# Performance work log

Measured on AMD Instinct MI355X. Metric: run time of the kernel, lower is better.

The kernel has to match this reference:

```python
import jax, jax.numpy as jnp
import numpy as np

H, W = 128, 128          # input_shape
OUT_H, OUT_W = 64, 64    # output_shape -> n_samples = 4096


def setup_inputs() -> dict:
    key = jax.random.key(0)
    k1, k2, k3 = jax.random.split(key, 3)
    activations = jax.random.normal(k1, (8, H, W), dtype=jnp.float32)
    mu = jax.random.uniform(k2, (OUT_H * OUT_W, 2), dtype=jnp.float32)
    sigma = jax.random.uniform(k3, (OUT_H * OUT_W, 2), dtype=jnp.float32)
    return {"activations": activations, "mu": mu, "sigma": sigma}


def reference(activations, mu, sigma):
    # coordinate grid: arange(dim)/dim per axis, range [0, 1)
    gh = jnp.arange(H, dtype=jnp.float32) / H          # [H]
    gw = jnp.arange(W, dtype=jnp.float32) / W          # [W]
    inv2s2 = 1.0 / (2.0 * jnp.square(sigma))           # [N, 2]
    # separable exponent: sum over dims splits into h-part + w-part
    eh = jnp.square(gh[:, None] - mu[None, :, 0]) * inv2s2[None, :, 0]  # [H, N]
    ew = jnp.square(gw[:, None] - mu[None, :, 1]) * inv2s2[None, :, 1]  # [W, N]
    pdf = jnp.exp(-(eh[:, None, :] + ew[None, :, :]))  # [H, W, N]
    # mean over spatial dims of pdf * activations (fused contraction)
    corr = jnp.einsum('bhw,hwn->bn', activations, pdf) / (H * W)  # [B, N]
    return corr.reshape(activations.shape[0], OUT_H, OUT_W)
```

## Files before the change

### kernel.cpp

```cpp
#include <hip/hip_runtime.h>

#define NOUT 4096
#define TN 32

typedef short bf16x8 __attribute__((ext_vector_type(8)));
typedef float f32x4  __attribute__((ext_vector_type(4)));

__device__ __forceinline__ unsigned short f2bf(float x) {
    unsigned u = __float_as_uint(x);
    u = (u + 0x7fffu + ((u >> 16) & 1u)) >> 16;
    return (unsigned short)u;
}
__device__ __forceinline__ float bf2f(unsigned short h) {
    return __uint_as_float(((unsigned)h) << 16);
}

__global__ __launch_bounds__(256) void gauss_mfma_kernel(
    const float* __restrict__ act,
    const float* __restrict__ mu,
    const float* __restrict__ sigma,
    float* __restrict__ out)
{
    __shared__ unsigned short EwH[32][136];
    __shared__ unsigned short EwL[32][136];
    __shared__ float4 musig[32];
    __shared__ float  red[4][32];

    const int t    = threadIdx.x;
    const int wv   = t >> 6;
    const int lane = t & 63;
    const int lm   = lane & 15;
    const int lg   = lane >> 4;
    const int n0   = blockIdx.x * TN;
    const int b    = blockIdx.y;
    const float* Ab = act + b * 16384;

    const float* rowA[2];
    rowA[0] = Ab + (wv * 32 + lm) * 128;
    rowA[1] = Ab + (wv * 32 + 16 + lm) * 128;
    float4 pre[2][2][2];
    #pragma unroll
    for (int ks = 0; ks < 2; ++ks)
        #pragma unroll
        for (int nh = 0; nh < 2; ++nh) {
            const float4* p = reinterpret_cast<const float4*>(rowA[nh] + ks * 32 + lg * 8);
            pre[ks][nh][0] = p[0];
            pre[ks][nh][1] = p[1];
        }

    if (t < TN) {
        float2 m = reinterpret_cast<const float2*>(mu)[n0 + t];
        float2 s = reinterpret_cast<const float2*>(sigma)[n0 + t];
        musig[t] = make_float4(m.x, m.y, 0.5f / (s.x * s.x), 0.5f / (s.y * s.y));
    }
    __syncthreads();

    #pragma unroll
    for (int r = 0; r < 8; ++r) {
        int p  = r * 256 + t;
        int n  = p >> 6;
        int wp = p & 63;
        float4 ms = musig[n];
        float g0 = (float)(2 * wp)     * (1.0f / 128.0f);
        float g1 = (float)(2 * wp + 1) * (1.0f / 128.0f);
        float d0 = g0 - ms.y, d1 = g1 - ms.y;
        float e0 = __expf(-d0 * d0 * ms.w);
        float e1 = __expf(-d1 * d1 * ms.w);
        unsigned short h0 = f2bf(e0), h1 = f2bf(e1);
        unsigned short l0 = f2bf(e0 - bf2f(h0)), l1 = f2bf(e1 - bf2f(h1));
        *reinterpret_cast<unsigned*>(&EwH[n][2 * wp]) = (unsigned)h0 | ((unsigned)h1 << 16);
        *reinterpret_cast<unsigned*>(&EwL[n][2 * wp]) = (unsigned)l0 | ((unsigned)l1 << 16);
    }
    __syncthreads();

    f32x4 acc[2][2] = {};
    #pragma unroll
    for (int ks = 0; ks < 4; ++ks) {
        const int cur = ks & 1;

        bf16x8 ahi[2], alo[2];
        #pragma unroll
        for (int nh = 0; nh < 2; ++nh) {
            float a[8] = { pre[cur][nh][0].x, pre[cur][nh][0].y, pre[cur][nh][0].z, pre[cur][nh][0].w,
                           pre[cur][nh][1].x, pre[cur][nh][1].y, pre[cur][nh][1].z, pre[cur][nh][1].w };
            #pragma unroll
            for (int j = 0; j < 8; ++j) {
                unsigned short hb = f2bf(a[j]);
                ahi[nh][j] = (short)hb;
                alo[nh][j] = (short)f2bf(a[j] - bf2f(hb));
            }
        }
        if (ks < 2) {
            #pragma unroll
            for (int nh = 0; nh < 2; ++nh) {
                const float4* p = reinterpret_cast<const float4*>(rowA[nh] + (ks + 2) * 32 + lg * 8);
                pre[cur][nh][0] = p[0];
                pre[cur][nh][1] = p[1];
            }
        }
        bf16x8 ewh[2], ewl[2];
        #pragma unroll
        for (int mf = 0; mf < 2; ++mf) {
            ewh[mf] = *reinterpret_cast<const bf16x8*>(&EwH[mf * 16 + lm][ks * 32 + lg * 8]);
            ewl[mf] = *reinterpret_cast<const bf16x8*>(&EwL[mf * 16 + lm][ks * 32 + lg * 8]);
        }
        #pragma unroll
        for (int mf = 0; mf < 2; ++mf)
            #pragma unroll
            for (int nh = 0; nh < 2; ++nh) {
                acc[mf][nh] = __builtin_amdgcn_mfma_f32_16x16x32_bf16(ewh[mf], ahi[nh], acc[mf][nh], 0, 0, 0);
                acc[mf][nh] = __builtin_amdgcn_mfma_f32_16x16x32_bf16(ewh[mf], alo[nh], acc[mf][nh], 0, 0, 0);
                acc[mf][nh] = __builtin_amdgcn_mfma_f32_16x16x32_bf16(ewl[mf], ahi[nh], acc[mf][nh], 0, 0, 0);
            }
    }

    const float gh0 = (float)(wv * 32 + lm)      * (1.0f / 128.0f);
    const float gh1 = (float)(wv * 32 + 16 + lm) * (1.0f / 128.0f);
    float s8[2][4];
    #pragma unroll
    for (int mf = 0; mf < 2; ++mf)
        #pragma unroll
        for (int r = 0; r < 4; ++r) {
            int n = mf * 16 + 4 * lg + r;
            float4 ms = musig[n];
            float d0 = gh0 - ms.x, d1 = gh1 - ms.x;
            float e0 = __expf(-d0 * d0 * ms.z);
            float e1 = __expf(-d1 * d1 * ms.z);
            float v = e0 * acc[mf][0][r] + e1 * acc[mf][1][r];
            v += __shfl_xor(v, 1, 64);
            v += __shfl_xor(v, 2, 64);
            v += __shfl_xor(v, 4, 64);
            v += __shfl_xor(v, 8, 64);
            s8[mf][r] = v;
        }
    if (lm == 0) {
        #pragma unroll
        for (int mf = 0; mf < 2; ++mf)
            #pragma unroll
            for (int r = 0; r < 4; ++r)
                red[wv][mf * 16 + 4 * lg + r] = s8[mf][r];
    }
    __syncthreads();

    if (t < TN) {
        float s = red[0][t] + red[1][t] + red[2][t] + red[3][t];
        out[b * NOUT + n0 + t] = s * (1.0f / 16384.0f);
    }
}

extern "C" void kernel_launch(void* const* d_in, const int* in_sizes, int n_in,
                              void* d_out, int out_size, void* d_ws, size_t ws_size,
                              hipStream_t stream) {
    const float* act   = (const float*)d_in[0];
    const float* mu    = (const float*)d_in[1];
    const float* sigma = (const float*)d_in[2];
    float* out = (float*)d_out;

    dim3 grid(NOUT / TN, 8);
    gauss_mfma_kernel<<<grid, 256, 0, stream>>>(act, mu, sigma, out);
}
```

Measured before the change: 16.16 us.

## Precompute fp16 hi/lo splits of activations and Ew in a prep kernel

Adds a prep kernel that splits the activations into fp16 hi/lo halves and computes the W-direction Gaussian factors, also as fp16 hi/lo, writing them to workspace in MFMA fragment order. The main kernel then loads these pre-split operands directly into LDS and registers and runs f16 MFMAs, with no per-block exp or conversion work. This removes work that was repeated across the 8 batch blocks and the 128 n-tiles. The cost is a second kernel launch plus a workspace round trip, and fp16 has a narrower exponent range than bf16, so small Gaussian values may lose accuracy.

```diff
diff --git a/kernel.cpp b/kernel.cpp
--- a/kernel.cpp
+++ b/kernel.cpp
@@ -1,28 +1,63 @@
 #include <hip/hip_runtime.h>
 
 #define NOUT 4096
-#define TN 32
+#define AH_OFF 0
+#define AL_OFF (256*1024)
+#define EW_OFF (512*1024)
 
-typedef short bf16x8 __attribute__((ext_vector_type(8)));
-typedef float f32x4  __attribute__((ext_vector_type(4)));
+typedef _Float16 f16x8 __attribute__((ext_vector_type(8)));
+typedef __fp16   h16x2 __attribute__((ext_vector_type(2)));
+typedef float    f32x4 __attribute__((ext_vector_type(4)));
 
-__device__ __forceinline__ unsigned short f2bf(float x) {
-    unsigned u = __float_as_uint(x);
-    u = (u + 0x7fffu + ((u >> 16) & 1u)) >> 16;
-    return (unsigned short)u;
-}
-__device__ __forceinline__ float bf2f(unsigned short h) {
-    return __uint_as_float(((unsigned)h) << 16);
+
+__global__ __launch_bounds__(256) void prep_kernel(
+    const float* __restrict__ act, const float* __restrict__ mu,
+    const float* __restrict__ sigma, char* __restrict__ ws)
+{
+    const int t = blockIdx.x * 256 + threadIdx.x;
+
+    float2 a = reinterpret_cast<const float2*>(act)[t];
+    h16x2 ahi = __builtin_amdgcn_cvt_pkrtz(a.x, a.y);
+    h16x2 alo = __builtin_amdgcn_cvt_pkrtz(a.x - (float)ahi[0], a.y - (float)ahi[1]);
+    reinterpret_cast<h16x2*>(ws + AH_OFF)[t] = ahi;
+    reinterpret_cast<h16x2*>(ws + AL_OFF)[t] = alo;
+
+    const int l    = t & 63;
+    float2 m, s;
+    {
+        const int mf   = (t >> 6) & 1;
+        const int tile = t >> 9;
+        const int n    = tile * 32 + mf * 16 + (l & 15);
+        m = reinterpret_cast<const float2*>(mu)[n];
+        s = reinterpret_cast<const float2*>(sigma)[n];
+    }
+    const int ks = (t >> 7) & 3;
+    const int w0 = ks * 32 + (l >> 4) * 8;
+    float inv = 0.5f / (s.y * s.y);
+    float e[8];
+    #pragma unroll
+    for (int j = 0; j < 8; ++j) {
+        float d = (float)(w0 + j) * (1.0f / 128.0f) - m.y;
+        e[j] = __expf(-d * d * inv);
+    }
+    f16x8 hi, lo;
+    #pragma unroll
+    for (int j = 0; j < 8; j += 2) {
+        h16x2 h2 = __builtin_amdgcn_cvt_pkrtz(e[j], e[j + 1]);
+        h16x2 l2 = __builtin_amdgcn_cvt_pkrtz(e[j] - (float)h2[0], e[j + 1] - (float)h2[1]);
+        hi[j] = (_Float16)(float)h2[0]; hi[j + 1] = (_Float16)(float)h2[1];
+        lo[j] = (_Float16)(float)l2[0]; lo[j + 1] = (_Float16)(float)l2[1];
+    }
+    char* base = ws + EW_OFF;
+    *reinterpret_cast<f16x8*>(base + (((size_t)(t >> 6) * 2 + 0) * 64 + l) * 16) = hi;
+    *reinterpret_cast<f16x8*>(base + (((size_t)(t >> 6) * 2 + 1) * 64 + l) * 16) = lo;
 }
 
-__global__ __launch_bounds__(256) void gauss_mfma_kernel(
-    const float* __restrict__ act,
-    const float* __restrict__ mu,
-    const float* __restrict__ sigma,
-    float* __restrict__ out)
+__global__ __launch_bounds__(256) void gauss_main_kernel(
+    const char* __restrict__ ws, const float* __restrict__ mu,
+    const float* __restrict__ sigma, float* __restrict__ out)
 {
-    __shared__ unsigned short EwH[32][136];
-    __shared__ unsigned short EwL[32][136];
+    __shared__ float4 EwLDS[1024];
     __shared__ float4 musig[32];
     __shared__ float  red[4][32];
 
@@ -31,91 +66,66 @@
     const int lane = t & 63;
     const int lm   = lane & 15;
     const int lg   = lane >> 4;
-    const int n0   = blockIdx.x * TN;
+    const int n0   = blockIdx.x * 32;
     const int b    = blockIdx.y;
-    const float* Ab = act + b * 16384;
 
-    const float* rowA[2];
-    rowA[0] = Ab + (wv * 32 + lm) * 128;
-    rowA[1] = Ab + (wv * 32 + 16 + lm) * 128;
-    float4 pre[2][2][2];
+    const float4* ewsrc = reinterpret_cast<const float4*>(ws + EW_OFF + (size_t)blockIdx.x * 16384);
+    float4 stg0 = ewsrc[t], stg1 = ewsrc[256 + t], stg2 = ewsrc[512 + t], stg3 = ewsrc[768 + t];
+
+    const _Float16* AH = reinterpret_cast<const _Float16*>(ws + AH_OFF);
+    const _Float16* AL = reinterpret_cast<const _Float16*>(ws + AL_OFF);
+    const int h0 = wv * 32 + lm, h1 = h0 + 16;
+    const _Float16* a0 = AH + ((b * 128 + h0) * 128 + lg * 8);
+    const _Float16* a1 = AH + ((b * 128 + h1) * 128 + lg * 8);
+    const _Float16* c0 = AL + ((b * 128 + h0) * 128 + lg * 8);
+    const _Float16* c1 = AL + ((b * 128 + h1) * 128 + lg * 8);
+
+    f16x8 pre[2][2][2];
     #pragma unroll
-    for (int ks = 0; ks < 2; ++ks)
-        #pragma unroll
-        for (int nh = 0; nh < 2; ++nh) {
-            const float4* p = reinterpret_cast<const float4*>(rowA[nh] + ks * 32 + lg * 8);
-            pre[ks][nh][0] = p[0];
-            pre[ks][nh][1] = p[1];
-        }
+    for (int s = 0; s < 2; ++s) {
+        pre[s][0][0] = *reinterpret_cast<const f16x8*>(a0 + s * 32);
+        pre[s][1][0] = *reinterpret_cast<const f16x8*>(a1 + s * 32);
+        pre[s][0][1] = *reinterpret_cast<const f16x8*>(c0 + s * 32);
+        pre[s][1][1] = *reinterpret_cast<const f16x8*>(c1 + s * 32);
+    }
 
-    if (t < TN) {
+    if (t < 32) {
         float2 m = reinterpret_cast<const float2*>(mu)[n0 + t];
         float2 s = reinterpret_cast<const float2*>(sigma)[n0 + t];
         musig[t] = make_float4(m.x, m.y, 0.5f / (s.x * s.x), 0.5f / (s.y * s.y));
     }
+
+    EwLDS[t] = stg0; EwLDS[256 + t] = stg1; EwLDS[512 + t] = stg2; EwLDS[768 + t] = stg3;
     __syncthreads();
 
-    #pragma unroll
-    for (int r = 0; r < 8; ++r) {
-        int p  = r * 256 + t;
-        int n  = p >> 6;
-        int wp = p & 63;
-        float4 ms = musig[n];
-        float g0 = (float)(2 * wp)     * (1.0f / 128.0f);
-        float g1 = (float)(2 * wp + 1) * (1.0f / 128.0f);
-        float d0 = g0 - ms.y, d1 = g1 - ms.y;
-        float e0 = __expf(-d0 * d0 * ms.w);
-        float e1 = __expf(-d1 * d1 * ms.w);
-        unsigned short h0 = f2bf(e0), h1 = f2bf(e1);
-        unsigned short l0 = f2bf(e0 - bf2f(h0)), l1 = f2bf(e1 - bf2f(h1));
-        *reinterpret_cast<unsigned*>(&EwH[n][2 * wp]) = (unsigned)h0 | ((unsigned)h1 << 16);
-        *reinterpret_cast<unsigned*>(&EwL[n][2 * wp]) = (unsigned)l0 | ((unsigned)l1 << 16);
-    }
-    __syncthreads();
-
+    const char* EwB = reinterpret_cast<const char*>(EwLDS);
     f32x4 acc[2][2] = {};
     #pragma unroll
     for (int ks = 0; ks < 4; ++ks) {
         const int cur = ks & 1;
-
-        bf16x8 ahi[2], alo[2];
-        #pragma unroll
-        for (int nh = 0; nh < 2; ++nh) {
-            float a[8] = { pre[cur][nh][0].x, pre[cur][nh][0].y, pre[cur][nh][0].z, pre[cur][nh][0].w,
-                           pre[cur][nh][1].x, pre[cur][nh][1].y, pre[cur][nh][1].z, pre[cur][nh][1].w };
-            #pragma unroll
-            for (int j = 0; j < 8; ++j) {
-                unsigned short hb = f2bf(a[j]);
-                ahi[nh][j] = (short)hb;
-                alo[nh][j] = (short)f2bf(a[j] - bf2f(hb));
-            }
+        f16x8 ah0 = pre[cur][0][0], ah1 = pre[cur][1][0];
+        f16x8 al0 = pre[cur][0][1], al1 = pre[cur][1][1];
+        if (ks < 2) {
+            pre[cur][0][0] = *reinterpret_cast<const f16x8*>(a0 + (ks + 2) * 32);
+            pre[cur][1][0] = *reinterpret_cast<const f16x8*>(a1 + (ks + 2) * 32);
+            pre[cur][0][1] = *reinterpret_cast<const f16x8*>(c0 + (ks + 2) * 32);
+            pre[cur][1][1] = *reinterpret_cast<const f16x8*>(c1 + (ks + 2) * 32);
         }
-        if (ks < 2) {
-            #pragma unroll
-            for (int nh = 0; nh < 2; ++nh) {
-                const float4* p = reinterpret_cast<const float4*>(rowA[nh] + (ks + 2) * 32 + lg * 8);
-                pre[cur][nh][0] = p[0];
-                pre[cur][nh][1] = p[1];
-            }
-        }
-        bf16x8 ewh[2], ewl[2];
         #pragma unroll
         for (int mf = 0; mf < 2; ++mf) {
-            ewh[mf] = *reinterpret_cast<const bf16x8*>(&EwH[mf * 16 + lm][ks * 32 + lg * 8]);
-            ewl[mf] = *reinterpret_cast<const bf16x8*>(&EwL[mf * 16 + lm][ks * 32 + lg * 8]);
+            f16x8 ewh = *reinterpret_cast<const f16x8*>(EwB + (((ks * 2 + mf) * 2 + 0) * 64 + lane) * 16);
+            f16x8 ewl = *reinterpret_cast<const f16x8*>(EwB + (((ks * 2 + mf) * 2 + 1) * 64 + lane) * 16);
+            acc[mf][0] = __builtin_amdgcn_mfma_f32_16x16x32_f16(ewh, ah0, acc[mf][0], 0, 0, 0);
+            acc[mf][0] = __builtin_amdgcn_mfma_f32_16x16x32_f16(ewh, al0, acc[mf][0], 0, 0, 0);
+            acc[mf][0] = __builtin_amdgcn_mfma_f32_16x16x32_f16(ewl, ah0, acc[mf][0], 0, 0, 0);
+            acc[mf][1] = __builtin_amdgcn_mfma_f32_16x16x32_f16(ewh, ah1, acc[mf][1], 0, 0, 0);
+            acc[mf][1] = __builtin_amdgcn_mfma_f32_16x16x32_f16(ewh, al1, acc[mf][1], 0, 0, 0);
+            acc[mf][1] = __builtin_amdgcn_mfma_f32_16x16x32_f16(ewl, ah1, acc[mf][1], 0, 0, 0);
         }
-        #pragma unroll
-        for (int mf = 0; mf < 2; ++mf)
-            #pragma unroll
-            for (int nh = 0; nh < 2; ++nh) {
-                acc[mf][nh] = __builtin_amdgcn_mfma_f32_16x16x32_bf16(ewh[mf], ahi[nh], acc[mf][nh], 0, 0, 0);
-                acc[mf][nh] = __builtin_amdgcn_mfma_f32_16x16x32_bf16(ewh[mf], alo[nh], acc[mf][nh], 0, 0, 0);
-                acc[mf][nh] = __builtin_amdgcn_mfma_f32_16x16x32_bf16(ewl[mf], ahi[nh], acc[mf][nh], 0, 0, 0);
-            }
     }
 
-    const float gh0 = (float)(wv * 32 + lm)      * (1.0f / 128.0f);
-    const float gh1 = (float)(wv * 32 + 16 + lm) * (1.0f / 128.0f);
+    const float gh0 = (float)h0 * (1.0f / 128.0f);
+    const float gh1 = (float)h1 * (1.0f / 128.0f);
     float s8[2][4];
     #pragma unroll
     for (int mf = 0; mf < 2; ++mf)
@@ -142,7 +152,7 @@
     }
     __syncthreads();
 
-    if (t < TN) {
+    if (t < 32) {
         float s = red[0][t] + red[1][t] + red[2][t] + red[3][t];
         out[b * NOUT + n0 + t] = s * (1.0f / 16384.0f);
     }
@@ -155,7 +165,9 @@
     const float* mu    = (const float*)d_in[1];
     const float* sigma = (const float*)d_in[2];
     float* out = (float*)d_out;
+    char* ws = (char*)d_ws;
 
-    dim3 grid(NOUT / TN, 8);
-    gauss_mfma_kernel<<<grid, 256, 0, stream>>>(act, mu, sigma, out);
+    prep_kernel<<<256, 256, 0, stream>>>(act, mu, sigma, ws);
+    dim3 grid(NOUT / 32, 8);
+    gauss_main_kernel<<<grid, 256, 0, stream>>>(ws, mu, sigma, out);
 }
```

Result: slower. 19.86 us (+22.9%).
